# Kernel optimization log

Measured on AMD Instinct MI355X. Metric: run time of the kernel, lower is better.

The kernel has to match this reference:

```python
import jax, jax.numpy as jnp
import numpy as np


def setup_inputs() -> dict:
    key = jax.random.key(0)
    B, C, N = 1, 8, 320
    n_shots, spp = 4, 1502
    inp = jax.random.normal(key, (B, C, N, N, 2), dtype=jnp.float32)
    # radial trajectory initialization, faithful to initilaize_trajectory('radial')
    theta = np.pi / n_shots
    L = np.arange(-160, 160, 320.0 / spp, dtype=np.float32)[:spp]
    traj = np.zeros((n_shots, spp, 2), dtype=np.float32)
    for i in range(n_shots):
        traj[i, :, 0] = L * np.cos(theta * i)
        traj[i, :, 1] = L * np.sin(theta * i)
    return {"inp": inp, "traj": jnp.asarray(traj)}


def _nufft_roundtrip(inp, traj):
    # inp: [B, C, H, W, 2] real/imag pairs; traj: [n_shots, spp, 2] in [-N/2, N/2)
    N = inp.shape[2]
    img = (inp[..., 0] + 1j * inp[..., 1]).astype(jnp.complex64)  # [B,C,H,W]
    xf = traj.reshape(-1, 2)                                      # [M,2]
    kx, ky = xf[:, 0], xf[:, 1]
    grid = (jnp.arange(N) - N // 2).astype(jnp.float32)           # centered pixel coords
    w = jnp.complex64(-2j * jnp.pi / N)
    Ax = jnp.exp(w * (kx[:, None] * grid[None, :])).astype(jnp.complex64)  # [M,H]
    Ay = jnp.exp(w * (ky[:, None] * grid[None, :])).astype(jnp.complex64)  # [M,W]
    # type-2 NUFFT (exact nonuniform DFT): image -> nonuniform k-space samples
    t = jnp.einsum('mx,bcxy->bcmy', Ax, img)        # [B,C,M,W]
    ksp = jnp.einsum('bcmy,my->bcm', t, Ay)         # [B,C,M]
    # adjoint (type-1): nonuniform samples -> Cartesian image grid
    tmp = ksp[..., None] * jnp.conj(Ay)[None, None]  # [B,C,M,W]
    out = jnp.einsum('mx,bcmw->bcxw', jnp.conj(Ax), tmp)  # [B,C,H,W]
    return jnp.stack([out.real, out.imag], axis=-1)  # [B,C,H,W,2]


def reference(inp, traj):
    return _nufft_roundtrip(inp, traj)
```

## Files before the change

### kernel.cpp

```cpp
#include <hip/hip_runtime.h>
#include <math.h>


#define NN      320
#define BCC     8
#define MREAL   6008
#define MSTR    6144
#define MT1     47
#define P1STR   6016
#define SKADJ   8
#define CHUNKM  (MSTR / SKADJ)
#define NADJB   1600
#define TWOPI   6.283185307179586f

typedef __attribute__((ext_vector_type(8))) short short8_t;
typedef __attribute__((ext_vector_type(4))) float float4_t;

__device__ __forceinline__ unsigned short f2bf(float f) {
    union { float f; unsigned u; } v; v.f = f;
    unsigned r = v.u + 0x7fff + ((v.u >> 16) & 1);
    return (unsigned short)(r >> 16);
}
__device__ __forceinline__ float bf2f(unsigned short h) {
    union { unsigned u; float f; } v; v.u = ((unsigned)h) << 16;
    return v.f;
}
__device__ __forceinline__ short8_t neg8(short8_t v) {
    short8_t r;
    #pragma unroll
    for (int i = 0; i < 8; ++i) r[i] = v[i] ^ (short)0x8000;
    return r;
}
__device__ __forceinline__ float gval(int i) { return (float)(i - NN/2); }

__device__ __forceinline__ void phase_cs(float k, float g, float* c, float* s) {
    float rev = k * (g * (1.0f / (float)NN));
    rev -= rintf(rev);
    float th = rev * TWOPI;
    __sincosf(th, s, c);
}

__global__ __launch_bounds__(256) void gen_A(
    const float* __restrict__ traj,
    unsigned short* __restrict__ Ax_r, unsigned short* __restrict__ Ax_i,
    unsigned short* __restrict__ AxT_r, unsigned short* __restrict__ AxT_i,
    unsigned short* __restrict__ AyT_r, unsigned short* __restrict__ AyT_i)
{
    __shared__ __align__(16) float lc[64][65];
    __shared__ __align__(16) float ls[64][65];
    __shared__ float kxv[64], kyv[64];
    const int tid = threadIdx.x;
    const int m0 = blockIdx.x * 64;
    const int g0 = blockIdx.y * 64;

    if (tid < 64) {
        int m = m0 + tid;
        kxv[tid] = (m < MREAL) ? traj[2*m]     : 0.f;
        kyv[tid] = (m < MREAL) ? traj[2*m + 1] : 0.f;
    }
    __syncthreads();

    #pragma unroll
    for (int it = 0; it < 16; ++it) {
        int e = tid + it * 256;
        int mi = e >> 6, gi = e & 63;
        float c, s;
        phase_cs(kxv[mi], gval(g0 + gi), &c, &s);
        bool valid = (m0 + mi) < MREAL;
        lc[mi][gi] = valid ? c : 0.f;
        ls[mi][gi] = valid ? s : 0.f;
    }
    __syncthreads();
    #pragma unroll
    for (int it = 0; it < 16; ++it) {
        int e = tid + it * 256;
        int mi = e >> 6, xi = e & 63;
        size_t o = (size_t)(m0 + mi) * NN + (g0 + xi);
        Ax_r[o] = f2bf(lc[mi][xi]);
        Ax_i[o] = f2bf(-ls[mi][xi]);
    }
    #pragma unroll
    for (int it = 0; it < 16; ++it) {
        int e = tid + it * 256;
        int xi = e >> 6, mi = e & 63;
        size_t o = (size_t)(g0 + xi) * MSTR + (m0 + mi);
        AxT_r[o] = f2bf(lc[mi][xi]);
        AxT_i[o] = f2bf(ls[mi][xi]);
    }
    __syncthreads();

    #pragma unroll
    for (int it = 0; it < 16; ++it) {
        int e = tid + it * 256;
        int mi = e >> 6, gi = e & 63;
        float c, s;
        phase_cs(kyv[mi], gval(g0 + gi), &c, &s);
        bool valid = (m0 + mi) < MREAL;
        lc[mi][gi] = valid ? c : 0.f;
        ls[mi][gi] = valid ? s : 0.f;
    }
    __syncthreads();
    #pragma unroll
    for (int it = 0; it < 16; ++it) {
        int e = tid + it * 256;
        int yi = e >> 6, mi = e & 63;
        size_t o = (size_t)(g0 + yi) * MSTR + (m0 + mi);
        AyT_r[o] = f2bf(lc[mi][yi]);
        AyT_i[o] = f2bf(ls[mi][yi]);
    }
}

__global__ __launch_bounds__(256) void conv_img(
    const float* __restrict__ inp,
    unsigned short* __restrict__ iT_r, unsigned short* __restrict__ iT_i)
{
    __shared__ __align__(16) float2 t[64][65];
    const int tid = threadIdx.x;
    const int x0 = blockIdx.x * 64, y0 = blockIdx.y * 64, bc = blockIdx.z;
    const float2* ip = (const float2*)inp;
    #pragma unroll
    for (int it = 0; it < 16; ++it) {
        int e = tid + it * 256;
        int r = e >> 6, c = e & 63;
        t[r][c] = ip[((size_t)bc * NN + (x0 + r)) * NN + (y0 + c)];
    }
    __syncthreads();
    #pragma unroll
    for (int it = 0; it < 16; ++it) {
        int e = tid + it * 256;
        int yy = e >> 6, xx = e & 63;
        float2 v = t[xx][yy];
        size_t o = ((size_t)bc * NN + (y0 + yy)) * NN + (x0 + xx);
        iT_r[o] = f2bf(v.x);
        iT_i[o] = f2bf(v.y);
    }
}

__global__ __launch_bounds__(256) void fwd_gemm(
    const unsigned short* __restrict__ iT_r, const unsigned short* __restrict__ iT_i,
    const unsigned short* __restrict__ Ax_r, const unsigned short* __restrict__ Ax_i,
    const unsigned short* __restrict__ AyT_r, const unsigned short* __restrict__ AyT_i,
    float2* __restrict__ partial1)
{
    __shared__ __align__(16) unsigned short Ar[64][72],  Ai[64][72];
    __shared__ __align__(16) unsigned short Br[128][72], Bi[128][72];
    __shared__ __align__(16) float2 redbuf[2][128];

    const int tid = threadIdx.x;
    const int bid = blockIdx.x;
    const int nid = (bid & 7) * 235 + (bid >> 3);
    const int mt  = nid / 40;
    const int r40 = nid - mt * 40;
    const int yt  = r40 % 5;
    const int bc  = r40 / 5;
    const int m0  = mt * 128;
    const int y0  = yt * 64;

    float4_t accR[2][4], accI[2][4];
    #pragma unroll
    for (int i = 0; i < 2; ++i)
        #pragma unroll
        for (int j = 0; j < 4; ++j) { accR[i][j] = (float4_t)0.f; accI[i][j] = (float4_t)0.f; }

    const int lane = tid & 63, wid = tid >> 6;
    const int wy = wid & 1, wm = wid >> 1;
    const int ar = lane & 15, kb = lane >> 4;

    const int row = tid >> 3;
    const int gr  = (tid & 7) * 8;

    const size_t ga0 = ((size_t)bc * NN + (y0 + row))      * NN + gr;
    const size_t ga1 = ((size_t)bc * NN + (y0 + row + 32)) * NN + gr;
    size_t gb[4];
    #pragma unroll
    for (int it = 0; it < 4; ++it) gb[it] = (size_t)(m0 + row + it * 32) * NN + gr;

    short8_t pAr0, pAr1, pAi0, pAi1;
    short8_t pBr0, pBr1, pBr2, pBr3, pBi0, pBi1, pBi2, pBi3;

#define FLOAD(xo) do { \
    pAr0 = *(const short8_t*)(iT_r + ga0 + (xo)); \
    pAi0 = *(const short8_t*)(iT_i + ga0 + (xo)); \
    pAr1 = *(const short8_t*)(iT_r + ga1 + (xo)); \
    pAi1 = *(const short8_t*)(iT_i + ga1 + (xo)); \
    pBr0 = *(const short8_t*)(Ax_r + gb[0] + (xo)); \
    pBi0 = *(const short8_t*)(Ax_i + gb[0] + (xo)); \
    pBr1 = *(const short8_t*)(Ax_r + gb[1] + (xo)); \
    pBi1 = *(const short8_t*)(Ax_i + gb[1] + (xo)); \
    pBr2 = *(const short8_t*)(Ax_r + gb[2] + (xo)); \
    pBi2 = *(const short8_t*)(Ax_i + gb[2] + (xo)); \
    pBr3 = *(const short8_t*)(Ax_r + gb[3] + (xo)); \
    pBi3 = *(const short8_t*)(Ax_i + gb[3] + (xo)); } while (0)

    FLOAD(0);
    for (int x0i = 0; x0i < NN; x0i += 64) {
        *(short8_t*)&Ar[row][gr]       = pAr0;
        *(short8_t*)&Ai[row][gr]       = pAi0;
        *(short8_t*)&Ar[row + 32][gr]  = pAr1;
        *(short8_t*)&Ai[row + 32][gr]  = pAi1;
        *(short8_t*)&Br[row][gr]       = pBr0;
        *(short8_t*)&Bi[row][gr]       = pBi0;
        *(short8_t*)&Br[row + 32][gr]  = pBr1;
        *(short8_t*)&Bi[row + 32][gr]  = pBi1;
        *(short8_t*)&Br[row + 64][gr]  = pBr2;
        *(short8_t*)&Bi[row + 64][gr]  = pBi2;
        *(short8_t*)&Br[row + 96][gr]  = pBr3;
        *(short8_t*)&Bi[row + 96][gr]  = pBi3;
        __syncthreads();

        if (x0i + 64 < NN) FLOAD(x0i + 64);

        #pragma unroll
        for (int ks = 0; ks < 2; ++ks) {
            short8_t a_r[2], a_i[2], a_n[2], b_r[4], b_i[4];
            #pragma unroll
            for (int iy = 0; iy < 2; ++iy) {
                int rr = wy * 32 + iy * 16 + ar;
                a_r[iy] = *(const short8_t*)&Ar[rr][ks * 32 + kb * 8];
                a_i[iy] = *(const short8_t*)&Ai[rr][ks * 32 + kb * 8];
                a_n[iy] = neg8(a_i[iy]);
            }
            #pragma unroll
            for (int jm = 0; jm < 4; ++jm) {
                int cc = wm * 64 + jm * 16 + ar;
                b_r[jm] = *(const short8_t*)&Br[cc][ks * 32 + kb * 8];
                b_i[jm] = *(const short8_t*)&Bi[cc][ks * 32 + kb * 8];
            }
            #pragma unroll
            for (int iy = 0; iy < 2; ++iy)
                #pragma unroll
                for (int jm = 0; jm < 4; ++jm) {
                    accR[iy][jm] = __builtin_amdgcn_mfma_f32_16x16x32_bf16(a_r[iy], b_r[jm], accR[iy][jm], 0, 0, 0);
                    accR[iy][jm] = __builtin_amdgcn_mfma_f32_16x16x32_bf16(a_n[iy], b_i[jm], accR[iy][jm], 0, 0, 0);
                    accI[iy][jm] = __builtin_amdgcn_mfma_f32_16x16x32_bf16(a_r[iy], b_i[jm], accI[iy][jm], 0, 0, 0);
                    accI[iy][jm] = __builtin_amdgcn_mfma_f32_16x16x32_bf16(a_i[iy], b_r[jm], accI[iy][jm], 0, 0, 0);
                }
        }
        __syncthreads();
    }
#undef FLOAD

    #pragma unroll
    for (int jm = 0; jm < 4; ++jm) {
        float sr = 0.f, si = 0.f;
        int m = m0 + wm * 64 + jm * 16 + ar;
        #pragma unroll
        for (int iy = 0; iy < 2; ++iy)
            #pragma unroll
            for (int q = 0; q < 4; ++q) {
                int y = y0 + wy * 32 + iy * 16 + kb * 4 + q;
                float c  = bf2f(AyT_r[(size_t)y * MSTR + m]);
                float sy = bf2f(AyT_i[(size_t)y * MSTR + m]);
                float Tr = accR[iy][jm][q], Ti = accI[iy][jm][q];
                sr += Tr * c + Ti * sy;
                si += Ti * c - Tr * sy;
            }
        sr += __shfl_xor(sr, 16); sr += __shfl_xor(sr, 32);
        si += __shfl_xor(si, 16); si += __shfl_xor(si, 32);
        if ((lane & 48) == 0)
            redbuf[wy][wm * 64 + jm * 16 + ar] = make_float2(sr, si);
    }
    __syncthreads();
    if (tid < 128) {
        float2 a = redbuf[0][tid], b = redbuf[1][tid];
        int m = m0 + tid;
        if (m < MREAL)
            partial1[((size_t)bc * 5 + yt) * P1STR + m] = make_float2(a.x + b.x, a.y + b.y);
    }
}

__global__ void reduce_ksp(const float2* __restrict__ partial1,
                           float2* __restrict__ ksp)
{
    int mp = blockIdx.x * 256 + threadIdx.x;
    int bc = blockIdx.y;
    float2 r = make_float2(0.f, 0.f);
    if (mp < MREAL) {
        #pragma unroll
        for (int yt = 0; yt < 5; ++yt) {
            float2 v = partial1[((size_t)bc * 5 + yt) * P1STR + mp];
            r.x += v.x; r.y += v.y;
        }
    }
    ksp[(size_t)bc * MSTR + mp] = r;
}

__global__ __launch_bounds__(256) void gen_U(
    const unsigned short* __restrict__ AyT_r, const unsigned short* __restrict__ AyT_i,
    const float2* __restrict__ ksp,
    unsigned short* __restrict__ U_r, unsigned short* __restrict__ U_i)
{
    const int tid = threadIdx.x;
    const int m0 = blockIdx.x * 2048 + tid * 8;
    const int y  = blockIdx.y;
    const int bc = blockIdx.z;

    short8_t yr = *(const short8_t*)(AyT_r + (size_t)y * MSTR + m0);
    short8_t yi = *(const short8_t*)(AyT_i + (size_t)y * MSTR + m0);
    const float2* kp = ksp + (size_t)bc * MSTR + m0;
    short8_t ur, ui;
    #pragma unroll
    for (int j = 0; j < 8; ++j) {
        float2 k = kp[j];
        float cr = bf2f((unsigned short)yr[j]);
        float ci = bf2f((unsigned short)yi[j]);
        ur[j] = (short)f2bf(k.x * cr - k.y * ci);
        ui[j] = (short)f2bf(k.x * ci + k.y * cr);
    }
    size_t o = ((size_t)bc * NN + y) * MSTR + m0;
    *(short8_t*)(U_r + o) = ur;
    *(short8_t*)(U_i + o) = ui;
}

template<int FP32P>
__global__ __launch_bounds__(256) void adj_gemm_pre(
    const unsigned short* __restrict__ AxT_r, const unsigned short* __restrict__ AxT_i,
    const unsigned short* __restrict__ U_r, const unsigned short* __restrict__ U_i,
    void* __restrict__ partial2)
{
    __shared__ __align__(16) unsigned short Ar[64][72], Ai[64][72];
    __shared__ __align__(16) unsigned short Br[64][72], Bi[64][72];

    const int tid = threadIdx.x;
    const int bid = blockIdx.x;
    const int nid = (bid & 7) * (NADJB / 8) + (bid >> 3);
    const int bcsk = nid / 25;
    const int xy = nid - bcsk * 25;
    const int xt = xy / 5, yt = xy % 5;
    const int bc = bcsk & 7, sk = bcsk >> 3;
    const int x0 = xt * 64, y0 = yt * 64;
    const int kbeg = sk * CHUNKM;

    float4_t accR[2][2], accI[2][2];
    #pragma unroll
    for (int i = 0; i < 2; ++i)
        #pragma unroll
        for (int j = 0; j < 2; ++j) { accR[i][j] = (float4_t)0.f; accI[i][j] = (float4_t)0.f; }

    const int lane = tid & 63, wid = tid >> 6;
    const int wx = wid >> 1, wyy = wid & 1;
    const int ar = lane & 15, kb = lane >> 4;

    const int row = tid >> 3;
    const int gr  = (tid & 7) * 8;

    const size_t ao0 = (size_t)(x0 + row)      * MSTR + kbeg + gr;
    const size_t ao1 = (size_t)(x0 + row + 32) * MSTR + kbeg + gr;
    const size_t bo0 = ((size_t)bc * NN + (y0 + row))      * MSTR + kbeg + gr;
    const size_t bo1 = ((size_t)bc * NN + (y0 + row + 32)) * MSTR + kbeg + gr;

    short8_t pAr0, pAr1, pAi0, pAi1, pBr0, pBr1, pBi0, pBi1;

#define ALOAD(mk) do { \
    pAr0 = *(const short8_t*)(AxT_r + ao0 + (mk)); \
    pAi0 = *(const short8_t*)(AxT_i + ao0 + (mk)); \
    pAr1 = *(const short8_t*)(AxT_r + ao1 + (mk)); \
    pAi1 = *(const short8_t*)(AxT_i + ao1 + (mk)); \
    pBr0 = *(const short8_t*)(U_r + bo0 + (mk)); \
    pBi0 = *(const short8_t*)(U_i + bo0 + (mk)); \
    pBr1 = *(const short8_t*)(U_r + bo1 + (mk)); \
    pBi1 = *(const short8_t*)(U_i + bo1 + (mk)); } while (0)

    ALOAD(0);
    for (int mk = 0; mk < CHUNKM; mk += 64) {
        *(short8_t*)&Ar[row][gr]      = pAr0;
        *(short8_t*)&Ai[row][gr]      = pAi0;
        *(short8_t*)&Ar[row + 32][gr] = pAr1;
        *(short8_t*)&Ai[row + 32][gr] = pAi1;
        *(short8_t*)&Br[row][gr]      = pBr0;
        *(short8_t*)&Bi[row][gr]      = pBi0;
        *(short8_t*)&Br[row + 32][gr] = pBr1;
        *(short8_t*)&Bi[row + 32][gr] = pBi1;
        __syncthreads();

        if (mk + 64 < CHUNKM) ALOAD(mk + 64);

        #pragma unroll
        for (int ks = 0; ks < 2; ++ks) {
            short8_t a_r[2], a_i[2], a_n[2], b_r[2], b_i[2];
            #pragma unroll
            for (int ix = 0; ix < 2; ++ix) {
                int rr = wx * 32 + ix * 16 + ar;
                a_r[ix] = *(const short8_t*)&Ar[rr][ks * 32 + kb * 8];
                a_i[ix] = *(const short8_t*)&Ai[rr][ks * 32 + kb * 8];
                a_n[ix] = neg8(a_i[ix]);
            }
            #pragma unroll
            for (int jy = 0; jy < 2; ++jy) {
                int cc = wyy * 32 + jy * 16 + ar;
                b_r[jy] = *(const short8_t*)&Br[cc][ks * 32 + kb * 8];
                b_i[jy] = *(const short8_t*)&Bi[cc][ks * 32 + kb * 8];
            }
            #pragma unroll
            for (int ix = 0; ix < 2; ++ix)
                #pragma unroll
                for (int jy = 0; jy < 2; ++jy) {
                    accR[ix][jy] = __builtin_amdgcn_mfma_f32_16x16x32_bf16(a_r[ix], b_r[jy], accR[ix][jy], 0, 0, 0);
                    accR[ix][jy] = __builtin_amdgcn_mfma_f32_16x16x32_bf16(a_n[ix], b_i[jy], accR[ix][jy], 0, 0, 0);
                    accI[ix][jy] = __builtin_amdgcn_mfma_f32_16x16x32_bf16(a_r[ix], b_i[jy], accI[ix][jy], 0, 0, 0);
                    accI[ix][jy] = __builtin_amdgcn_mfma_f32_16x16x32_bf16(a_i[ix], b_r[jy], accI[ix][jy], 0, 0, 0);
                }
        }
        __syncthreads();
    }
#undef ALOAD

    #pragma unroll
    for (int ix = 0; ix < 2; ++ix)
        #pragma unroll
        for (int jy = 0; jy < 2; ++jy)
            #pragma unroll
            for (int q = 0; q < 4; ++q) {
                int x = x0 + wx * 32 + ix * 16 + kb * 4 + q;
                int y = y0 + wyy * 32 + jy * 16 + ar;
                size_t o = (((size_t)sk * BCC + bc) * NN + x) * NN + y;
                float vr = accR[ix][jy][q], vi = accI[ix][jy][q];
                if (FP32P) {
                    ((float2*)partial2)[o] = make_float2(vr, vi);
                } else {
                    ((unsigned*)partial2)[o] =
                        (unsigned)f2bf(vr) | ((unsigned)f2bf(vi) << 16);
                }
            }
}

template<int FP32P>
__global__ __launch_bounds__(256) void adj_gemm_fb(
    const unsigned short* __restrict__ AxT_r, const unsigned short* __restrict__ AxT_i,
    const unsigned short* __restrict__ AyT_r, const unsigned short* __restrict__ AyT_i,
    const float2* __restrict__ ksp, void* __restrict__ partial2)
{
    __shared__ __align__(16) unsigned short Ar[64][72], Ai[64][72];
    __shared__ __align__(16) unsigned short Br[64][72], Bi[64][72];
    __shared__ __align__(16) float2 kspl[CHUNKM];

    const int tid = threadIdx.x;
    const int bid = blockIdx.x;
    const int nid = (bid & 7) * (NADJB / 8) + (bid >> 3);
    const int bcsk = nid / 25;
    const int xy = nid - bcsk * 25;
    const int xt = xy / 5, yt = xy % 5;
    const int bc = bcsk & 7, sk = bcsk >> 3;
    const int x0 = xt * 64, y0 = yt * 64;
    const int kbeg = sk * CHUNKM;

    #pragma unroll
    for (int it = 0; it < CHUNKM / 256; ++it)
        kspl[tid + it * 256] = ksp[(size_t)bc * MSTR + kbeg + tid + it * 256];
    __syncthreads();

    float4_t accR[2][2], accI[2][2];
    #pragma unroll
    for (int i = 0; i < 2; ++i)
        #pragma unroll
        for (int j = 0; j < 2; ++j) { accR[i][j] = (float4_t)0.f; accI[i][j] = (float4_t)0.f; }

    const int lane = tid & 63, wid = tid >> 6;
    const int wx = wid >> 1, wyy = wid & 1;
    const int ar = lane & 15, kb = lane >> 4;

    for (int mk = 0; mk < CHUNKM; mk += 64) {
        #pragma unroll
        for (int it = 0; it < 2; ++it) {
            int e = tid + it * 256;
            int row = e >> 3, gr = e & 7;
            size_t o = (size_t)(x0 + row) * MSTR + kbeg + mk + gr * 8;
            *(short8_t*)&Ar[row][gr * 8] = *(const short8_t*)(AxT_r + o);
            *(short8_t*)&Ai[row][gr * 8] = *(const short8_t*)(AxT_i + o);
        }
        #pragma unroll
        for (int it = 0; it < 2; ++it) {
            int e = tid + it * 256;
            int row = e >> 3, gr = e & 7;
            size_t o = (size_t)(y0 + row) * MSTR + kbeg + mk + gr * 8;
            short8_t yr = *(const short8_t*)(AyT_r + o);
            short8_t yi = *(const short8_t*)(AyT_i + o);
            short8_t br, bi2;
            #pragma unroll
            for (int j = 0; j < 8; ++j) {
                float2 k = kspl[mk + gr * 8 + j];
                float cr = bf2f((unsigned short)yr[j]);
                float ci = bf2f((unsigned short)yi[j]);
                br[j]  = (short)f2bf(k.x * cr - k.y * ci);
                bi2[j] = (short)f2bf(k.x * ci + k.y * cr);
            }
            *(short8_t*)&Br[row][gr * 8] = br;
            *(short8_t*)&Bi[row][gr * 8] = bi2;
        }
        __syncthreads();

        #pragma unroll
        for (int ks = 0; ks < 2; ++ks) {
            short8_t a_r[2], a_i[2], a_n[2], b_r[2], b_i[2];
            #pragma unroll
            for (int ix = 0; ix < 2; ++ix) {
                int rr = wx * 32 + ix * 16 + ar;
                a_r[ix] = *(const short8_t*)&Ar[rr][ks * 32 + kb * 8];
                a_i[ix] = *(const short8_t*)&Ai[rr][ks * 32 + kb * 8];
                a_n[ix] = neg8(a_i[ix]);
            }
            #pragma unroll
            for (int jy = 0; jy < 2; ++jy) {
                int cc = wyy * 32 + jy * 16 + ar;
                b_r[jy] = *(const short8_t*)&Br[cc][ks * 32 + kb * 8];
                b_i[jy] = *(const short8_t*)&Bi[cc][ks * 32 + kb * 8];
            }
            #pragma unroll
            for (int ix = 0; ix < 2; ++ix)
                #pragma unroll
                for (int jy = 0; jy < 2; ++jy) {
                    accR[ix][jy] = __builtin_amdgcn_mfma_f32_16x16x32_bf16(a_r[ix], b_r[jy], accR[ix][jy], 0, 0, 0);
                    accR[ix][jy] = __builtin_amdgcn_mfma_f32_16x16x32_bf16(a_n[ix], b_i[jy], accR[ix][jy], 0, 0, 0);
                    accI[ix][jy] = __builtin_amdgcn_mfma_f32_16x16x32_bf16(a_r[ix], b_i[jy], accI[ix][jy], 0, 0, 0);
                    accI[ix][jy] = __builtin_amdgcn_mfma_f32_16x16x32_bf16(a_i[ix], b_r[jy], accI[ix][jy], 0, 0, 0);
                }
        }
        __syncthreads();
    }

    #pragma unroll
    for (int ix = 0; ix < 2; ++ix)
        #pragma unroll
        for (int jy = 0; jy < 2; ++jy)
            #pragma unroll
            for (int q = 0; q < 4; ++q) {
                int x = x0 + wx * 32 + ix * 16 + kb * 4 + q;
                int y = y0 + wyy * 32 + jy * 16 + ar;
                size_t o = (((size_t)sk * BCC + bc) * NN + x) * NN + y;
                float vr = accR[ix][jy][q], vi = accI[ix][jy][q];
                if (FP32P) {
                    ((float2*)partial2)[o] = make_float2(vr, vi);
                } else {
                    ((unsigned*)partial2)[o] =
                        (unsigned)f2bf(vr) | ((unsigned)f2bf(vi) << 16);
                }
            }
}

template<int FP32P>
__global__ void reduce_out(const void* __restrict__ partial2,
                           float2* __restrict__ out)
{
    size_t total = (size_t)BCC * NN * NN;
    size_t idx = (size_t)blockIdx.x * 256 + threadIdx.x;
    if (idx >= total) return;
    float2 r = make_float2(0.f, 0.f);
    #pragma unroll
    for (int s = 0; s < SKADJ; ++s) {
        if (FP32P) {
            float2 v = ((const float2*)partial2)[s * total + idx];
            r.x += v.x; r.y += v.y;
        } else {
            unsigned u = ((const unsigned*)partial2)[s * total + idx];
            r.x += bf2f((unsigned short)(u & 0xffff));
            r.y += bf2f((unsigned short)(u >> 16));
        }
    }
    out[idx] = r;
}

extern "C" void kernel_launch(void* const* d_in, const int* in_sizes, int n_in,
                              void* d_out, int out_size, void* d_ws, size_t ws_size,
                              hipStream_t stream)
{
    const float* inp  = (const float*)d_in[0];
    const float* traj = (const float*)d_in[1];

    char* ws = (char*)d_ws;
    const size_t PL = (size_t)NN * MSTR * 2;
    unsigned short* AxT_r = (unsigned short*)(ws);
    unsigned short* AxT_i = (unsigned short*)(ws + PL);
    unsigned short* AyT_r = (unsigned short*)(ws + 2 * PL);
    unsigned short* AyT_i = (unsigned short*)(ws + 3 * PL);
    float2* ksp = (float2*)(ws + 4 * PL);
    const size_t KSPB = (size_t)BCC * MSTR * 8;
    const size_t BASE = 4 * PL + KSPB;
    char* rb = ws + BASE;
    unsigned short* Ax_r = (unsigned short*)(rb);
    unsigned short* Ax_i = (unsigned short*)(rb + PL);
    const size_t ITP = (size_t)BCC * NN * NN * 2;
    unsigned short* iT_r = (unsigned short*)(rb + 2 * PL);
    unsigned short* iT_i = (unsigned short*)(rb + 2 * PL + ITP);
    float2* partial1 = (float2*)(rb + 2 * PL + 2 * ITP);
    const size_t UPL = (size_t)BCC * NN * MSTR * 2;
    unsigned short* U_r = (unsigned short*)(rb);
    unsigned short* U_i = (unsigned short*)(rb + UPL);
    const size_t ADJ_F32 = (size_t)SKADJ * BCC * NN * NN * 8;
    const size_t ADJ_B16 = ADJ_F32 / 2;

    gen_A<<<dim3(96, 5), 256, 0, stream>>>(traj, Ax_r, Ax_i, AxT_r, AxT_i, AyT_r, AyT_i);
    conv_img<<<dim3(5, 5, BCC), 256, 0, stream>>>(inp, iT_r, iT_i);
    fwd_gemm<<<dim3(1880), 256, 0, stream>>>(iT_r, iT_i, Ax_r, Ax_i, AyT_r, AyT_i, partial1);
    reduce_ksp<<<dim3(24, BCC), 256, 0, stream>>>(partial1, ksp);

    size_t total = (size_t)BCC * NN * NN;
    int rblocks = (int)((total + 255) / 256);

    if (ws_size >= BASE + 2 * UPL + ADJ_F32) {
        void* partial2 = (void*)(rb + 2 * UPL);
        gen_U<<<dim3(3, NN, BCC), 256, 0, stream>>>(AyT_r, AyT_i, ksp, U_r, U_i);
        adj_gemm_pre<1><<<dim3(NADJB), 256, 0, stream>>>(AxT_r, AxT_i, U_r, U_i, partial2);
        reduce_out<1><<<rblocks, 256, 0, stream>>>(partial2, (float2*)d_out);
    } else if (ws_size >= BASE + 2 * UPL + ADJ_B16) {
        void* partial2 = (void*)(rb + 2 * UPL);
        gen_U<<<dim3(3, NN, BCC), 256, 0, stream>>>(AyT_r, AyT_i, ksp, U_r, U_i);
        adj_gemm_pre<0><<<dim3(NADJB), 256, 0, stream>>>(AxT_r, AxT_i, U_r, U_i, partial2);
        reduce_out<0><<<rblocks, 256, 0, stream>>>(partial2, (float2*)d_out);
    } else if (ws_size >= BASE + ADJ_F32) {
        void* partial2 = (void*)rb;
        adj_gemm_fb<1><<<dim3(NADJB), 256, 0, stream>>>(AxT_r, AxT_i, AyT_r, AyT_i, ksp, partial2);
        reduce_out<1><<<rblocks, 256, 0, stream>>>(partial2, (float2*)d_out);
    } else {
        void* partial2 = (void*)rb;
        adj_gemm_fb<0><<<dim3(NADJB), 256, 0, stream>>>(AxT_r, AxT_i, AyT_r, AyT_i, ksp, partial2);
        reduce_out<0><<<rblocks, 256, 0, stream>>>(partial2, (float2*)d_out);
    }
}
```

Measured before the change: 144.3 us.

## Load A operand directly from global into registers, drop LDS A tiles, fewer split-K chunks

In the forward and adjoint GEMM kernels, the A operand fragments are now read straight from global memory into MFMA registers instead of being staged through shared memory. This removes the LDS tiles for A and lowers shared-memory use, with launch bounds added so more blocks can reside per CU. The adjoint split-K factor drops from 8 to 6, which means fewer blocks and less partial-sum traffic but longer K loops. The A loads are no longer prefetched a step ahead and are issued right before the MFMAs, so global latency may be exposed.

```diff
diff --git a/kernel.cpp b/kernel.cpp
--- a/kernel.cpp
+++ b/kernel.cpp
@@ -8,9 +8,9 @@
 #define MSTR    6144
 #define MT1     47
 #define P1STR   6016
-#define SKADJ   8
+#define SKADJ   6
 #define CHUNKM  (MSTR / SKADJ)
-#define NADJB   1600
+#define NADJB   (SKADJ * BCC * 25)
 #define TWOPI   6.283185307179586f
 
 typedef __attribute__((ext_vector_type(8))) short short8_t;
@@ -136,13 +136,12 @@
     }
 }
 
-__global__ __launch_bounds__(256) void fwd_gemm(
+__global__ __launch_bounds__(256, 4) void fwd_gemm(
     const unsigned short* __restrict__ iT_r, const unsigned short* __restrict__ iT_i,
     const unsigned short* __restrict__ Ax_r, const unsigned short* __restrict__ Ax_i,
     const unsigned short* __restrict__ AyT_r, const unsigned short* __restrict__ AyT_i,
     float2* __restrict__ partial1)
 {
-    __shared__ __align__(16) unsigned short Ar[64][72],  Ai[64][72];
     __shared__ __align__(16) unsigned short Br[128][72], Bi[128][72];
     __shared__ __align__(16) float2 redbuf[2][128];
 
@@ -169,20 +168,18 @@
     const int row = tid >> 3;
     const int gr  = (tid & 7) * 8;
 
-    const size_t ga0 = ((size_t)bc * NN + (y0 + row))      * NN + gr;
-    const size_t ga1 = ((size_t)bc * NN + (y0 + row + 32)) * NN + gr;
     size_t gb[4];
     #pragma unroll
     for (int it = 0; it < 4; ++it) gb[it] = (size_t)(m0 + row + it * 32) * NN + gr;
 
-    short8_t pAr0, pAr1, pAi0, pAi1;
+    size_t aoff[2];
+    #pragma unroll
+    for (int iy = 0; iy < 2; ++iy)
+        aoff[iy] = ((size_t)bc * NN + (y0 + wy * 32 + iy * 16 + ar)) * NN + kb * 8;
+
     short8_t pBr0, pBr1, pBr2, pBr3, pBi0, pBi1, pBi2, pBi3;
 
-#define FLOAD(xo) do { \
-    pAr0 = *(const short8_t*)(iT_r + ga0 + (xo)); \
-    pAi0 = *(const short8_t*)(iT_i + ga0 + (xo)); \
-    pAr1 = *(const short8_t*)(iT_r + ga1 + (xo)); \
-    pAi1 = *(const short8_t*)(iT_i + ga1 + (xo)); \
+#define BLOAD(xo) do { \
     pBr0 = *(const short8_t*)(Ax_r + gb[0] + (xo)); \
     pBi0 = *(const short8_t*)(Ax_i + gb[0] + (xo)); \
     pBr1 = *(const short8_t*)(Ax_r + gb[1] + (xo)); \
@@ -192,12 +189,8 @@
     pBr3 = *(const short8_t*)(Ax_r + gb[3] + (xo)); \
     pBi3 = *(const short8_t*)(Ax_i + gb[3] + (xo)); } while (0)
 
-    FLOAD(0);
+    BLOAD(0);
     for (int x0i = 0; x0i < NN; x0i += 64) {
-        *(short8_t*)&Ar[row][gr]       = pAr0;
-        *(short8_t*)&Ai[row][gr]       = pAi0;
-        *(short8_t*)&Ar[row + 32][gr]  = pAr1;
-        *(short8_t*)&Ai[row + 32][gr]  = pAi1;
         *(short8_t*)&Br[row][gr]       = pBr0;
         *(short8_t*)&Bi[row][gr]       = pBi0;
         *(short8_t*)&Br[row + 32][gr]  = pBr1;
@@ -208,16 +201,15 @@
         *(short8_t*)&Bi[row + 96][gr]  = pBi3;
         __syncthreads();
 
-        if (x0i + 64 < NN) FLOAD(x0i + 64);
+        if (x0i + 64 < NN) BLOAD(x0i + 64);
 
         #pragma unroll
         for (int ks = 0; ks < 2; ++ks) {
             short8_t a_r[2], a_i[2], a_n[2], b_r[4], b_i[4];
             #pragma unroll
             for (int iy = 0; iy < 2; ++iy) {
-                int rr = wy * 32 + iy * 16 + ar;
-                a_r[iy] = *(const short8_t*)&Ar[rr][ks * 32 + kb * 8];
-                a_i[iy] = *(const short8_t*)&Ai[rr][ks * 32 + kb * 8];
+                a_r[iy] = *(const short8_t*)(iT_r + aoff[iy] + x0i + ks * 32);
+                a_i[iy] = *(const short8_t*)(iT_i + aoff[iy] + x0i + ks * 32);
                 a_n[iy] = neg8(a_i[iy]);
             }
             #pragma unroll
@@ -238,7 +230,7 @@
         }
         __syncthreads();
     }
-#undef FLOAD
+#undef BLOAD
 
     #pragma unroll
     for (int jm = 0; jm < 4; ++jm) {
@@ -313,12 +305,11 @@
 }
 
 template<int FP32P>
-__global__ __launch_bounds__(256) void adj_gemm_pre(
+__global__ __launch_bounds__(256, 5) void adj_gemm_pre(
     const unsigned short* __restrict__ AxT_r, const unsigned short* __restrict__ AxT_i,
     const unsigned short* __restrict__ U_r, const unsigned short* __restrict__ U_i,
     void* __restrict__ partial2)
 {
-    __shared__ __align__(16) unsigned short Ar[64][72], Ai[64][72];
     __shared__ __align__(16) unsigned short Br[64][72], Bi[64][72];
 
     const int tid = threadIdx.x;
@@ -327,7 +318,7 @@
     const int bcsk = nid / 25;
     const int xy = nid - bcsk * 25;
     const int xt = xy / 5, yt = xy % 5;
-    const int bc = bcsk & 7, sk = bcsk >> 3;
+    const int bc = bcsk % BCC, sk = bcsk / BCC;
     const int x0 = xt * 64, y0 = yt * 64;
     const int kbeg = sk * CHUNKM;
 
@@ -344,45 +335,39 @@
     const int row = tid >> 3;
     const int gr  = (tid & 7) * 8;
 
-    const size_t ao0 = (size_t)(x0 + row)      * MSTR + kbeg + gr;
-    const size_t ao1 = (size_t)(x0 + row + 32) * MSTR + kbeg + gr;
     const size_t bo0 = ((size_t)bc * NN + (y0 + row))      * MSTR + kbeg + gr;
     const size_t bo1 = ((size_t)bc * NN + (y0 + row + 32)) * MSTR + kbeg + gr;
 
-    short8_t pAr0, pAr1, pAi0, pAi1, pBr0, pBr1, pBi0, pBi1;
-
-#define ALOAD(mk) do { \
-    pAr0 = *(const short8_t*)(AxT_r + ao0 + (mk)); \
-    pAi0 = *(const short8_t*)(AxT_i + ao0 + (mk)); \
-    pAr1 = *(const short8_t*)(AxT_r + ao1 + (mk)); \
-    pAi1 = *(const short8_t*)(AxT_i + ao1 + (mk)); \
+    size_t aoff[2];
+    #pragma unroll
+    for (int ix = 0; ix < 2; ++ix)
+        aoff[ix] = (size_t)(x0 + wx * 32 + ix * 16 + ar) * MSTR + kbeg + kb * 8;
+
+    short8_t pBr0, pBr1, pBi0, pBi1;
+
+#define BLOAD(mk) do { \
     pBr0 = *(const short8_t*)(U_r + bo0 + (mk)); \
     pBi0 = *(const short8_t*)(U_i + bo0 + (mk)); \
     pBr1 = *(const short8_t*)(U_r + bo1 + (mk)); \
     pBi1 = *(const short8_t*)(U_i + bo1 + (mk)); } while (0)
 
-    ALOAD(0);
+    BLOAD(0);
     for (int mk = 0; mk < CHUNKM; mk += 64) {
-        *(short8_t*)&Ar[row][gr]      = pAr0;
-        *(short8_t*)&Ai[row][gr]      = pAi0;
-        *(short8_t*)&Ar[row + 32][gr] = pAr1;
-        *(short8_t*)&Ai[row + 32][gr] = pAi1;
         *(short8_t*)&Br[row][gr]      = pBr0;
         *(short8_t*)&Bi[row][gr]      = pBi0;
         *(short8_t*)&Br[row + 32][gr] = pBr1;
         *(short8_t*)&Bi[row + 32][gr] = pBi1;
         __syncthreads();
 
-        if (mk + 64 < CHUNKM) ALOAD(mk + 64);
+        if (mk + 64 < CHUNKM) BLOAD(mk + 64);
 
         #pragma unroll
         for (int ks = 0; ks < 2; ++ks) {
             short8_t a_r[2], a_i[2], a_n[2], b_r[2], b_i[2];
             #pragma unroll
             for (int ix = 0; ix < 2; ++ix) {
-                int rr = wx * 32 + ix * 16 + ar;
-                a_r[ix] = *(const short8_t*)&Ar[rr][ks * 32 + kb * 8];
-                a_i[ix] = *(const short8_t*)&Ai[rr][ks * 32 + kb * 8];
+                a_r[ix] = *(const short8_t*)(AxT_r + aoff[ix] + mk + ks * 32);
+                a_i[ix] = *(const short8_t*)(AxT_i + aoff[ix] + mk + ks * 32);
                 a_n[ix] = neg8(a_i[ix]);
             }
             #pragma unroll
@@ -403,7 +388,7 @@
         }
         __syncthreads();
     }
-#undef ALOAD
+#undef BLOAD
 
     #pragma unroll
     for (int ix = 0; ix < 2; ++ix)
@@ -440,7 +425,7 @@
     const int bcsk = nid / 25;
     const int xy = nid - bcsk * 25;
     const int xt = xy / 5, yt = xy % 5;
-    const int bc = bcsk & 7, sk = bcsk >> 3;
+    const int bc = bcsk % BCC, sk = bcsk / BCC;
     const int x0 = xt * 64, y0 = yt * 64;
     const int kbeg = sk * CHUNKM;
 
```

Measured after the change: 374.7 us. 160% more time.
